# Performance work log

Hardware: AMD Instinct MI355X
Metric: run time of the kernel (lower is better)

Reference implementation:

```python
import jax, jax.numpy as jnp
import numpy as np

SIGMA = 5.0  # matches init_kwargs sigma


def so3_exp_map(w):
    """Rodrigues formula. w: [..., 3] axis-angle -> [..., 3, 3] rotation."""
    theta = jnp.sqrt(jnp.sum(w * w, axis=-1) + 1e-12)            # [...]
    wx, wy, wz = w[..., 0], w[..., 1], w[..., 2]
    z = jnp.zeros_like(wx)
    # normalized skew matrix K = hat(w) / theta
    K = jnp.stack([z, -wz, wy,
                   wz, z, -wx,
                   -wy, wx, z], axis=-1).reshape(w.shape[:-1] + (3, 3))
    K = K / theta[..., None, None]
    s = jnp.sin(theta)[..., None, None]
    c = (1.0 - jnp.cos(theta))[..., None, None]
    I = jnp.eye(3, dtype=w.dtype)
    return I + s * K + c * (K @ K)


def setup_inputs() -> dict:
    key = jax.random.key(0)
    k1, k2, k3, k4, k5 = jax.random.split(key, 5)
    P, N, E = 65536, 512, 4096
    # spread points/control points over a volume where sigma=5 is a meaningful scale
    points = jax.random.normal(k1, (P, 3), dtype=jnp.float32) * 10.0
    control_points = jax.random.normal(k2, (N, 3), dtype=jnp.float32) * 10.0
    rot_vec = jax.random.normal(k3, (N, 3), dtype=jnp.float32) * 0.1
    t = jax.random.normal(k4, (N, 3), dtype=jnp.float32) * 0.1
    edges = jax.random.randint(k5, (E, 2), 0, N, dtype=jnp.int64)
    return {"points": points, "control_points": control_points,
            "rot_vec": rot_vec, "t": t, "edges": edges}


def reference(points, control_points, rot_vec, t, edges):
    # ---- warp_points ----
    # local: [P, N, 3]
    local = points[:, None, :] - control_points[None, :, :]
    skin = jnp.exp(-jnp.sum(local * local, axis=-1) / (2.0 * SIGMA * SIGMA))  # [P, N]
    skin = skin / (jnp.sum(skin, axis=-1, keepdims=True) + 1e-5)
    R = so3_exp_map(rot_vec)                                    # [N, 3, 3]
    warped = (jnp.einsum('nij,pnj->pni', R, local)
              + t[None, :, :] + control_points[None, :, :])     # [P, N, 3]
    warped = jnp.sum(warped * skin[..., None], axis=1)          # [P, 3]
    # ---- reg_term ----
    i, j = edges[:, 0], edges[:, 1]
    ci, cj = control_points[i], control_points[j]               # [E, 3]
    ti, tj = t[i], t[j]
    Ri = R[i]                                                   # [E, 3, 3]
    resid = jnp.einsum('mij,mj->mi', Ri, cj - ci) + ci + ti - (cj + tj)
    reg = jnp.sum(resid * resid)
    return warped, reg
```

## Files before the change

kernel.cpp:

```cpp
#include <hip/hip_runtime.h>
#include <math.h>


constexpr int NP = 65536;
constexpr int PPB = 256;
constexpr float KEXP = -0.02f * 1.44269504088896340736f;
constexpr float M2K  = -2.0f * KEXP;
constexpr float WLOG = 10.0f;
constexpr float EPSS = 1e-5f * 1024.0f;
constexpr float INV2PI = 0.15915494309189535f;

typedef _Float16 half8 __attribute__((ext_vector_type(8)));
typedef float    f32x4 __attribute__((ext_vector_type(4)));

__device__ __forceinline__ float fast_exp2(float x) {
    float r; asm("v_exp_f32 %0, %1" : "=v"(r) : "v"(x)); return r;
}
__device__ __forceinline__ float fast_sin2pi(float x) {
    float r; asm("v_sin_f32 %0, %1" : "=v"(r) : "v"(x)); return r;
}
__device__ __forceinline__ float fast_cos2pi(float x) {
    float r; asm("v_cos_f32 %0, %1" : "=v"(r) : "v"(x)); return r;
}

__device__ __forceinline__ void rodrigues(float wx, float wy, float wz, float* R) {
    float t2 = wx * wx + wy * wy + wz * wz + 1e-12f;
    float th = sqrtf(t2);
    float inv = 1.0f / th;
    float kx = wx * inv, ky = wy * inv, kz = wz * inv;
    float rev = th * INV2PI;
    float s = fast_sin2pi(rev);
    float c = 1.0f - fast_cos2pi(rev);
    float kxky = kx * ky, kxkz = kx * kz, kykz = ky * kz;
    R[0] = 1.0f - c * (ky * ky + kz * kz);
    R[1] = -s * kz + c * kxky;
    R[2] =  s * ky + c * kxkz;
    R[3] =  s * kz + c * kxky;
    R[4] = 1.0f - c * (kx * kx + kz * kz);
    R[5] = -s * kx + c * kykz;
    R[6] = -s * ky + c * kxkz;
    R[7] =  s * kx + c * kykz;
    R[8] = 1.0f - c * (kx * kx + ky * ky);
}

__global__ __launch_bounds__(512, 2) void deform_kernel(
    const float* __restrict__ points,
    const float* __restrict__ cps,
    const float* __restrict__ rot,
    const float* __restrict__ tr,
    const int* __restrict__ edges,
    float* __restrict__ out)
{
    __shared__ float4 ndp[576];
    __shared__ half8 tf[16][64];
    __shared__ float cs[4][2][4][16][17];

    const int tid = threadIdx.x;
    const int bid = blockIdx.x;

    const int lane = tid & 63;
    const int wv   = tid >> 6;
    const int rg   = wv >> 1;
    const int kh   = wv & 1;
    const int m    = lane & 15;
    const int bq   = lane >> 4;

    const int pbase = bid * PPB + rg * 64 + m;
    float px[4], py[4], pz[4], kp2[4];
    #pragma unroll
    for (int t = 0; t < 4; ++t) {
        int p = pbase + t * 16;
        px[t] = points[3 * p];
        py[t] = points[3 * p + 1];
        pz[t] = points[3 * p + 2];
        kp2[t] = KEXP * (px[t] * px[t] + py[t] * py[t] + pz[t] * pz[t]);
    }

    {
        const int n = tid;
        float R[9];
        rodrigues(rot[3 * n], rot[3 * n + 1], rot[3 * n + 2], R);
        float cx = cps[3 * n], cy = cps[3 * n + 1], cz = cps[3 * n + 2];
        float tx = tr[3 * n],  ty = tr[3 * n + 1],  tz = tr[3 * n + 2];
        float bx = tx + cx - (R[0] * cx + R[1] * cy + R[2] * cz);
        float by = ty + cy - (R[3] * cx + R[4] * cy + R[5] * cz);
        float bz = tz + cz - (R[6] * cx + R[7] * cy + R[8] * cz);
        ndp[n + (n >> 3)] = make_float4(M2K * cx, M2K * cy, M2K * cz,
                                        KEXP * (cx * cx + cy * cy + cz * cz) + WLOG);
        const int ks = n >> 5, rr = n & 31, b = rr >> 3, j = rr & 7;
        _Float16* tb = ((_Float16*)&tf[ks][16 * b]) + j;
        tb[0 * 8]  = (_Float16)R[0];
        tb[1 * 8]  = (_Float16)R[1];
        tb[2 * 8]  = (_Float16)R[2];
        tb[3 * 8]  = (_Float16)R[3];
        tb[4 * 8]  = (_Float16)R[4];
        tb[5 * 8]  = (_Float16)R[5];
        tb[6 * 8]  = (_Float16)R[6];
        tb[7 * 8]  = (_Float16)R[7];
        tb[8 * 8]  = (_Float16)R[8];
        tb[9 * 8]  = (_Float16)bx;
        tb[10 * 8] = (_Float16)by;
        tb[11 * 8] = (_Float16)bz;
        tb[12 * 8] = (_Float16)1.0f;
        tb[13 * 8] = (_Float16)0.0f;
        tb[14 * 8] = (_Float16)0.0f;
        tb[15 * 8] = (_Float16)0.0f;
    }
    __syncthreads();

    f32x4 acc[4] = {{0,0,0,0}, {0,0,0,0}, {0,0,0,0}, {0,0,0,0}};

    #pragma unroll 2
    for (int ks = kh * 8; ks < kh * 8 + 8; ++ks) {
        half8 bf = tf[ks][lane];
        const float4* cqp = &ndp[ks * 36 + bq * 9];
        float4 cq[8];
        #pragma unroll
        for (int j = 0; j < 8; ++j) cq[j] = cqp[j];

        #pragma unroll
        for (int t = 0; t < 4; ++t) {
            float w[8];
            #pragma unroll
            for (int j = 0; j < 8; ++j)
                w[j] = fast_exp2(fmaf(cq[j].x, px[t],
                                 fmaf(cq[j].y, py[t],
                                 fmaf(cq[j].z, pz[t], kp2[t] + cq[j].w))));
            union { half8 v; unsigned int u[4]; } a;
            #pragma unroll
            for (int q = 0; q < 4; ++q)
                a.u[q] = __builtin_bit_cast(unsigned int,
                             __builtin_amdgcn_cvt_pkrtz(w[2 * q], w[2 * q + 1]));
            acc[t] = __builtin_amdgcn_mfma_f32_16x16x32_f16(a.v, bf, acc[t], 0, 0, 0);
        }
    }

    #pragma unroll
    for (int t = 0; t < 4; ++t)
        #pragma unroll
        for (int jj = 0; jj < 4; ++jj)
            cs[rg][kh][t][bq * 4 + jj][m] = acc[t][jj];
    __syncthreads();

    if (tid < PPB) {
        const int p = bid * PPB + tid;
        const int rg2 = tid >> 6, w2 = tid & 63, t2 = w2 >> 4, m2 = w2 & 15;
        float c[13];
        #pragma unroll
        for (int i = 0; i < 13; ++i)
            c[i] = cs[rg2][0][t2][m2][i] + cs[rg2][1][t2][m2][i];
        float qx = points[3 * p], qy = points[3 * p + 1], qz = points[3 * p + 2];
        float inv = 1.0f / (c[12] + EPSS);
        float ox = fmaf(c[0], qx, fmaf(c[1], qy, fmaf(c[2], qz, c[9])))  * inv;
        float oy = fmaf(c[3], qx, fmaf(c[4], qy, fmaf(c[5], qz, c[10]))) * inv;
        float oz = fmaf(c[6], qx, fmaf(c[7], qy, fmaf(c[8], qz, c[11]))) * inv;
        out[3 * p + 0] = ox;
        out[3 * p + 1] = oy;
        out[3 * p + 2] = oz;
    } else if (tid < PPB + 16) {
        const int e = bid * 16 + (tid - PPB);
        const int i  = edges[2 * e + 0];
        const int j2 = edges[2 * e + 1];
        float Ri[9];
        rodrigues(rot[3 * i], rot[3 * i + 1], rot[3 * i + 2], Ri);
        float cix = cps[3 * i], ciy = cps[3 * i + 1], ciz = cps[3 * i + 2];
        float cjx = cps[3 * j2], cjy = cps[3 * j2 + 1], cjz = cps[3 * j2 + 2];
        float dx = cjx - cix, dy = cjy - ciy, dz = cjz - ciz;
        float rx = fmaf(Ri[0], dx, fmaf(Ri[1], dy, Ri[2] * dz)) + cix + tr[3 * i + 0] - cjx - tr[3 * j2 + 0];
        float ry = fmaf(Ri[3], dx, fmaf(Ri[4], dy, Ri[5] * dz)) + ciy + tr[3 * i + 1] - cjy - tr[3 * j2 + 1];
        float rz = fmaf(Ri[6], dx, fmaf(Ri[7], dy, Ri[8] * dz)) + ciz + tr[3 * i + 2] - cjz - tr[3 * j2 + 2];
        float acc2 = rx * rx + ry * ry + rz * rz;
        #pragma unroll
        for (int off = 8; off > 0; off >>= 1)
            acc2 += __shfl_down(acc2, off, 16);
        if (tid == PPB) atomicAdd(out + 3 * NP, acc2);
    }
}

extern "C" void kernel_launch(void* const* d_in, const int* in_sizes, int n_in,
                              void* d_out, int out_size, void* d_ws, size_t ws_size,
                              hipStream_t stream) {
    const float* points = (const float*)d_in[0];
    const float* cps    = (const float*)d_in[1];
    const float* rot    = (const float*)d_in[2];
    const float* tr     = (const float*)d_in[3];
    const int*   edges  = (const int*)d_in[4];
    float* out = (float*)d_out;
    deform_kernel<<<NP / PPB, 512, 0, stream>>>(points, cps, rot, tr, edges, out);
}
```

Baseline: 73.39 us.

## Move edge regularizer to dedicated block and pack point FMAs into float2

The edge residual reduction moves out of the 256 point blocks into one extra block. That block loops over all edges, reduces them with wave shuffles and shared memory, and writes the scalar directly, so per-block atomics go away. The inner skinning loop now computes the exp arguments for point pairs using two-wide vector FMAs, meant to map onto packed FP32 instructions and cut VALU count. The extra block runs its whole edge loop serially in one block and may become a tail on the critical path.

Measured after the change: 73.39 us. About the same (-0.0%).

```diff
diff --git a/kernel.cpp b/kernel.cpp
--- a/kernel.cpp
+++ b/kernel.cpp
@@ -4,6 +4,7 @@
 
 constexpr int NP = 65536;
 constexpr int PPB = 256;
+constexpr int NE = 4096;
 constexpr float KEXP = -0.02f * 1.44269504088896340736f;
 constexpr float M2K  = -2.0f * KEXP;
 constexpr float WLOG = 10.0f;
@@ -12,6 +13,7 @@
 
 typedef _Float16 half8 __attribute__((ext_vector_type(8)));
 typedef float    f32x4 __attribute__((ext_vector_type(4)));
+typedef float    f32x2 __attribute__((ext_vector_type(2)));
 
 __device__ __forceinline__ float fast_exp2(float x) {
     float r; asm("v_exp_f32 %0, %1" : "=v"(r) : "v"(x)); return r;
@@ -22,6 +24,10 @@
 __device__ __forceinline__ float fast_cos2pi(float x) {
     float r; asm("v_cos_f32 %0, %1" : "=v"(r) : "v"(x)); return r;
 }
+__device__ __forceinline__ f32x2 fm2(f32x2 a, f32x2 b, f32x2 c) {
+    return __builtin_elementwise_fma(a, b, c);
+}
+__device__ __forceinline__ f32x2 sp2(float s) { f32x2 r; r.x = s; r.y = s; return r; }
 
 __device__ __forceinline__ void rodrigues(float wx, float wy, float wz, float* R) {
     float t2 = wx * wx + wy * wy + wz * wz + 1e-12f;
@@ -54,126 +60,161 @@
     __shared__ float4 ndp[576];
     __shared__ half8 tf[16][64];
     __shared__ float cs[4][2][4][16][17];
+    __shared__ float redE[8];
 
     const int tid = threadIdx.x;
     const int bid = blockIdx.x;
 
-    const int lane = tid & 63;
-    const int wv   = tid >> 6;
-    const int rg   = wv >> 1;
-    const int kh   = wv & 1;
-    const int m    = lane & 15;
-    const int bq   = lane >> 4;
-
-    const int pbase = bid * PPB + rg * 64 + m;
-    float px[4], py[4], pz[4], kp2[4];
-    #pragma unroll
-    for (int t = 0; t < 4; ++t) {
-        int p = pbase + t * 16;
-        px[t] = points[3 * p];
-        py[t] = points[3 * p + 1];
-        pz[t] = points[3 * p + 2];
-        kp2[t] = KEXP * (px[t] * px[t] + py[t] * py[t] + pz[t] * pz[t]);
-    }
-
-    {
-        const int n = tid;
-        float R[9];
-        rodrigues(rot[3 * n], rot[3 * n + 1], rot[3 * n + 2], R);
-        float cx = cps[3 * n], cy = cps[3 * n + 1], cz = cps[3 * n + 2];
-        float tx = tr[3 * n],  ty = tr[3 * n + 1],  tz = tr[3 * n + 2];
-        float bx = tx + cx - (R[0] * cx + R[1] * cy + R[2] * cz);
-        float by = ty + cy - (R[3] * cx + R[4] * cy + R[5] * cz);
-        float bz = tz + cz - (R[6] * cx + R[7] * cy + R[8] * cz);
-        ndp[n + (n >> 3)] = make_float4(M2K * cx, M2K * cy, M2K * cz,
-                                        KEXP * (cx * cx + cy * cy + cz * cz) + WLOG);
-        const int ks = n >> 5, rr = n & 31, b = rr >> 3, j = rr & 7;
-        _Float16* tb = ((_Float16*)&tf[ks][16 * b]) + j;
-        tb[0 * 8]  = (_Float16)R[0];
-        tb[1 * 8]  = (_Float16)R[1];
-        tb[2 * 8]  = (_Float16)R[2];
-        tb[3 * 8]  = (_Float16)R[3];
-        tb[4 * 8]  = (_Float16)R[4];
-        tb[5 * 8]  = (_Float16)R[5];
-        tb[6 * 8]  = (_Float16)R[6];
-        tb[7 * 8]  = (_Float16)R[7];
-        tb[8 * 8]  = (_Float16)R[8];
-        tb[9 * 8]  = (_Float16)bx;
-        tb[10 * 8] = (_Float16)by;
-        tb[11 * 8] = (_Float16)bz;
-        tb[12 * 8] = (_Float16)1.0f;
-        tb[13 * 8] = (_Float16)0.0f;
-        tb[14 * 8] = (_Float16)0.0f;
-        tb[15 * 8] = (_Float16)0.0f;
-    }
-    __syncthreads();
-
-    f32x4 acc[4] = {{0,0,0,0}, {0,0,0,0}, {0,0,0,0}, {0,0,0,0}};
-
-    #pragma unroll 2
-    for (int ks = kh * 8; ks < kh * 8 + 8; ++ks) {
-        half8 bf = tf[ks][lane];
-        const float4* cqp = &ndp[ks * 36 + bq * 9];
-        float4 cq[8];
-        #pragma unroll
-        for (int j = 0; j < 8; ++j) cq[j] = cqp[j];
-
+    if (bid < NP / PPB) {
+        const int lane = tid & 63;
+        const int wv   = tid >> 6;
+        const int rg   = wv >> 1;
+        const int kh   = wv & 1;
+        const int m    = lane & 15;
+        const int bq   = lane >> 4;
+
+        const int pbase = bid * PPB + rg * 64 + m;
+        float px[4], py[4], pz[4], kp2[4];
         #pragma unroll
         for (int t = 0; t < 4; ++t) {
-            float w[8];
-            #pragma unroll
-            for (int j = 0; j < 8; ++j)
-                w[j] = fast_exp2(fmaf(cq[j].x, px[t],
-                                 fmaf(cq[j].y, py[t],
-                                 fmaf(cq[j].z, pz[t], kp2[t] + cq[j].w))));
+            int p = pbase + t * 16;
+            px[t] = points[3 * p];
+            py[t] = points[3 * p + 1];
+            pz[t] = points[3 * p + 2];
+            kp2[t] = KEXP * (px[t] * px[t] + py[t] * py[t] + pz[t] * pz[t]);
+        }
+
+        {
+            const int n = tid;
+            float R[9];
+            rodrigues(rot[3 * n], rot[3 * n + 1], rot[3 * n + 2], R);
+            float cx = cps[3 * n], cy = cps[3 * n + 1], cz = cps[3 * n + 2];
+            float tx = tr[3 * n],  ty = tr[3 * n + 1],  tz = tr[3 * n + 2];
+            float bx = tx + cx - (R[0] * cx + R[1] * cy + R[2] * cz);
+            float by = ty + cy - (R[3] * cx + R[4] * cy + R[5] * cz);
+            float bz = tz + cz - (R[6] * cx + R[7] * cy + R[8] * cz);
+            ndp[n + (n >> 3)] = make_float4(M2K * cx, M2K * cy, M2K * cz,
+                                            KEXP * (cx * cx + cy * cy + cz * cz) + WLOG);
+            const int ks = n >> 5, rr = n & 31, b = rr >> 3, j = rr & 7;
+            _Float16* tb = ((_Float16*)&tf[ks][16 * b]) + j;
+            tb[0 * 8]  = (_Float16)R[0];
+            tb[1 * 8]  = (_Float16)R[1];
+            tb[2 * 8]  = (_Float16)R[2];
+            tb[3 * 8]  = (_Float16)R[3];
+            tb[4 * 8]  = (_Float16)R[4];
+            tb[5 * 8]  = (_Float16)R[5];
+            tb[6 * 8]  = (_Float16)R[6];
+            tb[7 * 8]  = (_Float16)R[7];
+            tb[8 * 8]  = (_Float16)R[8];
+            tb[9 * 8]  = (_Float16)bx;
+            tb[10 * 8] = (_Float16)by;
+            tb[11 * 8] = (_Float16)bz;
+            tb[12 * 8] = (_Float16)1.0f;
+            tb[13 * 8] = (_Float16)0.0f;
+            tb[14 * 8] = (_Float16)0.0f;
+            tb[15 * 8] = (_Float16)0.0f;
+        }
+        __syncthreads();
+
+        f32x2 Px01 = {px[0], px[1]}, Px23 = {px[2], px[3]};
+        f32x2 Py01 = {py[0], py[1]}, Py23 = {py[2], py[3]};
+        f32x2 Pz01 = {pz[0], pz[1]}, Pz23 = {pz[2], pz[3]};
+        f32x2 K01  = {kp2[0], kp2[1]}, K23 = {kp2[2], kp2[3]};
+
+        f32x4 acc[4] = {{0,0,0,0}, {0,0,0,0}, {0,0,0,0}, {0,0,0,0}};
+
+        #pragma unroll 2
+        for (int ks = kh * 8; ks < kh * 8 + 8; ++ks) {
+            half8 bf = tf[ks][lane];
+            const float4* cqp = &ndp[ks * 36 + bq * 9];
+            float w0[8], w1[8], w2[8], w3[8];
+            #pragma unroll
+            for (int j = 0; j < 8; ++j) {
+                float4 cq = cqp[j];
+                f32x2 cw = sp2(cq.w);
+                f32x2 a01 = fm2(sp2(cq.x), Px01,
+                            fm2(sp2(cq.y), Py01,
+                            fm2(sp2(cq.z), Pz01, K01 + cw)));
+                f32x2 a23 = fm2(sp2(cq.x), Px23,
+                            fm2(sp2(cq.y), Py23,
+                            fm2(sp2(cq.z), Pz23, K23 + cw)));
+                w0[j] = fast_exp2(a01.x);
+                w1[j] = fast_exp2(a01.y);
+                w2[j] = fast_exp2(a23.x);
+                w3[j] = fast_exp2(a23.y);
+            }
             union { half8 v; unsigned int u[4]; } a;
             #pragma unroll
             for (int q = 0; q < 4; ++q)
                 a.u[q] = __builtin_bit_cast(unsigned int,
-                             __builtin_amdgcn_cvt_pkrtz(w[2 * q], w[2 * q + 1]));
-            acc[t] = __builtin_amdgcn_mfma_f32_16x16x32_f16(a.v, bf, acc[t], 0, 0, 0);
-        }
-    }
-
-    #pragma unroll
-    for (int t = 0; t < 4; ++t)
+                             __builtin_amdgcn_cvt_pkrtz(w0[2 * q], w0[2 * q + 1]));
+            acc[0] = __builtin_amdgcn_mfma_f32_16x16x32_f16(a.v, bf, acc[0], 0, 0, 0);
+            #pragma unroll
+            for (int q = 0; q < 4; ++q)
+                a.u[q] = __builtin_bit_cast(unsigned int,
+                             __builtin_amdgcn_cvt_pkrtz(w1[2 * q], w1[2 * q + 1]));
+            acc[1] = __builtin_amdgcn_mfma_f32_16x16x32_f16(a.v, bf, acc[1], 0, 0, 0);
+            #pragma unroll
+            for (int q = 0; q < 4; ++q)
+                a.u[q] = __builtin_bit_cast(unsigned int,
+                             __builtin_amdgcn_cvt_pkrtz(w2[2 * q], w2[2 * q + 1]));
+            acc[2] = __builtin_amdgcn_mfma_f32_16x16x32_f16(a.v, bf, acc[2], 0, 0, 0);
+            #pragma unroll
+            for (int q = 0; q < 4; ++q)
+                a.u[q] = __builtin_bit_cast(unsigned int,
+                             __builtin_amdgcn_cvt_pkrtz(w3[2 * q], w3[2 * q + 1]));
+            acc[3] = __builtin_amdgcn_mfma_f32_16x16x32_f16(a.v, bf, acc[3], 0, 0, 0);
+        }
+
         #pragma unroll
-        for (int jj = 0; jj < 4; ++jj)
-            cs[rg][kh][t][bq * 4 + jj][m] = acc[t][jj];
-    __syncthreads();
-
-    if (tid < PPB) {
-        const int p = bid * PPB + tid;
-        const int rg2 = tid >> 6, w2 = tid & 63, t2 = w2 >> 4, m2 = w2 & 15;
-        float c[13];
+        for (int t = 0; t < 4; ++t)
+            #pragma unroll
+            for (int jj = 0; jj < 4; ++jj)
+                cs[rg][kh][t][bq * 4 + jj][m] = acc[t][jj];
+        __syncthreads();
+
+        if (tid < PPB) {
+            const int p = bid * PPB + tid;
+            const int rg2 = tid >> 6, w2 = tid & 63, t2 = w2 >> 4, m2 = w2 & 15;
+            float c[13];
+            #pragma unroll
+            for (int i = 0; i < 13; ++i)
+                c[i] = cs[rg2][0][t2][m2][i] + cs[rg2][1][t2][m2][i];
+            float qx = points[3 * p], qy = points[3 * p + 1], qz = points[3 * p + 2];
+            float inv = 1.0f / (c[12] + EPSS);
+            float ox = fmaf(c[0], qx, fmaf(c[1], qy, fmaf(c[2], qz, c[9])))  * inv;
+            float oy = fmaf(c[3], qx, fmaf(c[4], qy, fmaf(c[5], qz, c[10]))) * inv;
+            float oz = fmaf(c[6], qx, fmaf(c[7], qy, fmaf(c[8], qz, c[11]))) * inv;
+            out[3 * p + 0] = ox;
+            out[3 * p + 1] = oy;
+            out[3 * p + 2] = oz;
+        }
+    } else {
+        float acc = 0.0f;
+        for (int e = tid; e < NE; e += 512) {
+            int i  = edges[2 * e + 0];
+            int j2 = edges[2 * e + 1];
+            float Ri[9];
+            rodrigues(rot[3 * i], rot[3 * i + 1], rot[3 * i + 2], Ri);
+            float cix = cps[3 * i], ciy = cps[3 * i + 1], ciz = cps[3 * i + 2];
+            float cjx = cps[3 * j2], cjy = cps[3 * j2 + 1], cjz = cps[3 * j2 + 2];
+            float dx = cjx - cix, dy = cjy - ciy, dz = cjz - ciz;
+            float rx = fmaf(Ri[0], dx, fmaf(Ri[1], dy, Ri[2] * dz)) + cix + tr[3 * i + 0] - cjx - tr[3 * j2 + 0];
+            float ry = fmaf(Ri[3], dx, fmaf(Ri[4], dy, Ri[5] * dz)) + ciy + tr[3 * i + 1] - cjy - tr[3 * j2 + 1];
+            float rz = fmaf(Ri[6], dx, fmaf(Ri[7], dy, Ri[8] * dz)) + ciz + tr[3 * i + 2] - cjz - tr[3 * j2 + 2];
+            acc += rx * rx + ry * ry + rz * rz;
+        }
         #pragma unroll
-        for (int i = 0; i < 13; ++i)
-            c[i] = cs[rg2][0][t2][m2][i] + cs[rg2][1][t2][m2][i];
-        float qx = points[3 * p], qy = points[3 * p + 1], qz = points[3 * p + 2];
-        float inv = 1.0f / (c[12] + EPSS);
-        float ox = fmaf(c[0], qx, fmaf(c[1], qy, fmaf(c[2], qz, c[9])))  * inv;
-        float oy = fmaf(c[3], qx, fmaf(c[4], qy, fmaf(c[5], qz, c[10]))) * inv;
-        float oz = fmaf(c[6], qx, fmaf(c[7], qy, fmaf(c[8], qz, c[11]))) * inv;
-        out[3 * p + 0] = ox;
-        out[3 * p + 1] = oy;
-        out[3 * p + 2] = oz;
-    } else if (tid < PPB + 16) {
-        const int e = bid * 16 + (tid - PPB);
-        const int i  = edges[2 * e + 0];
-        const int j2 = edges[2 * e + 1];
-        float Ri[9];
-        rodrigues(rot[3 * i], rot[3 * i + 1], rot[3 * i + 2], Ri);
-        float cix = cps[3 * i], ciy = cps[3 * i + 1], ciz = cps[3 * i + 2];
-        float cjx = cps[3 * j2], cjy = cps[3 * j2 + 1], cjz = cps[3 * j2 + 2];
-        float dx = cjx - cix, dy = cjy - ciy, dz = cjz - ciz;
-        float rx = fmaf(Ri[0], dx, fmaf(Ri[1], dy, Ri[2] * dz)) + cix + tr[3 * i + 0] - cjx - tr[3 * j2 + 0];
-        float ry = fmaf(Ri[3], dx, fmaf(Ri[4], dy, Ri[5] * dz)) + ciy + tr[3 * i + 1] - cjy - tr[3 * j2 + 1];
-        float rz = fmaf(Ri[6], dx, fmaf(Ri[7], dy, Ri[8] * dz)) + ciz + tr[3 * i + 2] - cjz - tr[3 * j2 + 2];
-        float acc2 = rx * rx + ry * ry + rz * rz;
-        #pragma unroll
-        for (int off = 8; off > 0; off >>= 1)
-            acc2 += __shfl_down(acc2, off, 16);
-        if (tid == PPB) atomicAdd(out + 3 * NP, acc2);
+        for (int off = 32; off > 0; off >>= 1)
+            acc += __shfl_down(acc, off, 64);
+        if ((tid & 63) == 0) redE[tid >> 6] = acc;
+        __syncthreads();
+        if (tid == 0) {
+            float s = 0.0f;
+            #pragma unroll
+            for (int i = 0; i < 8; ++i) s += redE[i];
+            out[3 * NP] = s;
+        }
     }
 }
 
@@ -186,5 +227,5 @@
     const float* tr     = (const float*)d_in[3];
     const int*   edges  = (const int*)d_in[4];
     float* out = (float*)d_out;
-    deform_kernel<<<NP / PPB, 512, 0, stream>>>(points, cps, rot, tr, edges, out);
-}
+    deform_kernel<<<NP / PPB + 1, 512, 0, stream>>>(points, cps, rot, tr, edges, out);
+}
```
